# Kernel tuning notes

Hardware: AMD Instinct MI355X
Metric: run time of the kernel (lower is better)

## Reference

```python
import jax, jax.numpy as jnp
import numpy as np
from jax import lax

DIM = 2048
HEAD_DIM = 128
N_HEADS = 16
N_KV_HEADS = 4
N_REP = N_HEADS // N_KV_HEADS
K_CHUNK = 8          # token_chunk
SEQ = 2048
BATCH = 1
ROPE_THETA = 10000.0
KV_DIM = N_KV_HEADS * HEAD_DIM  # 512


def _make_freq_cis(seq, hd, theta):
    # (seq, hd//2, 2, 2) rotation matrices [[cos, -sin], [sin, cos]]
    inv = 1.0 / (theta ** (np.arange(0, hd, 2, dtype=np.float64) / hd))
    ang = np.outer(np.arange(seq, dtype=np.float64), inv)
    cos, sin = np.cos(ang), np.sin(ang)
    f = np.stack([np.stack([cos, -sin], -1), np.stack([sin, cos], -1)], -2)
    return jnp.asarray(f, jnp.float32)


def setup_inputs() -> dict:
    key = jax.random.key(0)
    ks = jax.random.split(key, 12)
    s = 0.02
    inp = {
        'x': jax.random.normal(ks[0], (BATCH, SEQ, DIM), jnp.float32),
        'freq_cis': _make_freq_cis(SEQ, HEAD_DIM, ROPE_THETA),
        # nn.Linear weights stored as (out, in); y = x @ W.T
        'wq': jax.random.normal(ks[1], (N_HEADS * HEAD_DIM, DIM), jnp.float32) * s,
        'wk': jax.random.normal(ks[2], (KV_DIM, DIM), jnp.float32) * s,
        'wv': jax.random.normal(ks[3], (KV_DIM, DIM), jnp.float32) * s,
        'wo': jax.random.normal(ks[4], (DIM, N_HEADS * HEAD_DIM), jnp.float32) * s,
        # diagonal SSM params for k_ssm / v_ssm (per-channel)
        'a_log_k': jax.random.normal(ks[5], (KV_DIM,), jnp.float32) * 0.5,
        'b_k': jax.random.normal(ks[6], (KV_DIM,), jnp.float32),
        'c_k': jax.random.normal(ks[7], (KV_DIM,), jnp.float32),
        'a_log_v': jax.random.normal(ks[8], (KV_DIM,), jnp.float32) * 0.5,
        'b_v': jax.random.normal(ks[9], (KV_DIM,), jnp.float32),
        'c_v': jax.random.normal(ks[10], (KV_DIM,), jnp.float32),
    }
    return inp


def _ssm_chunked(x, a_log, b, c):
    # Chunked diagonal SSM with state reset every K_CHUNK tokens
    # (equivalent to flat_process_chunks_with_ssm with boundaries every K).
    bsz, S, E = x.shape
    nc = S // K_CHUNK
    a = jnp.exp(-jax.nn.softplus(a_log))  # (E,) decay in (0, 1)
    xs = x.reshape(bsz * nc, K_CHUNK, E).swapaxes(0, 1)  # (K, N, E)

    def step(h, xt):
        h = a * h + b * xt
        return h, c * h

    _, ys = lax.scan(step, jnp.zeros((bsz * nc, E), x.dtype), xs)
    return ys.swapaxes(0, 1).reshape(bsz, S, E)


def _apply_rope(xq, xk, freq_cis):
    # xq: (b, s, h, hd); freq_cis: (s, hd//2, 2, 2)
    def rot(t):
        b, s, h, hd = t.shape
        tr = t.reshape(b, s, h, hd // 2, 1, 2)
        f = freq_cis.reshape(1, s, 1, hd // 2, 2, 2)
        return (tr * f).sum(-1).reshape(b, s, h, hd)
    return rot(xq), rot(xk)


def _forward(x, freq_cis, wq, wk, wv, wo, a_log_k, b_k, c_k, a_log_v, b_v, c_v):
    bsz, S, _ = x.shape
    xq = jnp.einsum('bsd,ed->bse', x, wq)
    xk = jnp.einsum('bsd,ed->bse', x, wk)
    xv = jnp.einsum('bsd,ed->bse', x, wv)

    # chunked SSM preprocessing of K/V (+ residual_ssm)
    xk_p = _ssm_chunked(xk, a_log_k, b_k, c_k) + xk
    xv_p = _ssm_chunked(xv, a_log_v, b_v, c_v) + xv

    xq = xq.reshape(bsz, S, N_HEADS, HEAD_DIM)
    xk_p = xk_p.reshape(bsz, S, N_KV_HEADS, HEAD_DIM)
    xv_p = xv_p.reshape(bsz, S, N_KV_HEADS, HEAD_DIM)

    xq, xk_p = _apply_rope(xq, xk_p, freq_cis)

    # GQA repeat_kv (torch.repeat_interleave on head dim)
    xk_p = jnp.repeat(xk_p, N_REP, axis=2)
    xv_p = jnp.repeat(xv_p, N_REP, axis=2)

    # chunk-boundary attention mask
    k_pos = jnp.arange(S)
    boundary = (k_pos % K_CHUNK) == (K_CHUNK - 1)
    t = jnp.arange(S)[:, None]
    k = k_pos[None, :]
    mask = ((k < t) & boundary[None, :]) | (k == t - 1) | ((k < 4) & (k <= t))

    q = xq.transpose(0, 2, 1, 3)   # (b, h, s, d)
    kk = xk_p.transpose(0, 2, 1, 3)
    vv = xv_p.transpose(0, 2, 1, 3)

    scores = jnp.einsum('bhqd,bhkd->bhqk', q, kk) / jnp.sqrt(
        jnp.asarray(HEAD_DIM, q.dtype))
    scores = jnp.where(mask[None, None], scores, -jnp.inf)
    attn = jax.nn.softmax(scores, axis=-1)
    out = jnp.einsum('bhqk,bhkd->bhqd', attn, vv)
    out = out.transpose(0, 2, 1, 3).reshape(bsz, S, N_HEADS * HEAD_DIM)
    return jnp.einsum('bse,de->bsd', out, wo)


def reference(x, freq_cis, wq, wk, wv, wo, a_log_k, b_k, c_k,
              a_log_v, b_v, c_v):
    return _forward(x, freq_cis, wq, wk, wv, wo,
                    a_log_k, b_k, c_k, a_log_v, b_v, c_v)
```

## Files before the change

kernel.cpp:

```cpp
#include <hip/hip_runtime.h>

typedef __bf16 bf16x8 __attribute__((ext_vector_type(8)));
typedef float  f32x4  __attribute__((ext_vector_type(4)));
typedef unsigned short u16;
typedef unsigned int   u32;

__device__ __forceinline__ float b2f(u16 u) {
    u32 x = ((u32)u) << 16;
    return __builtin_bit_cast(float, x);
}
__device__ __forceinline__ u16 f2b(float f) {
    u32 x = __builtin_bit_cast(u32, f);
    x += 0x7fffu + ((x >> 16) & 1u);
    return (u16)(x >> 16);
}

__global__ void convert_kernel(const float* __restrict__ x, const float* __restrict__ wq,
                               const float* __restrict__ wk, const float* __restrict__ wv,
                               const float* __restrict__ wo,
                               u16* __restrict__ xb, u16* __restrict__ wcat, u16* __restrict__ wob)
{
    long i4 = (long)blockIdx.x * 256 + threadIdx.x;
    long e = i4 * 4;
    const float* src; u16* dst;
    if (e < 4194304) { src = x + e; dst = xb + e; }
    else if (e < 10485760) {
        long j = e - 4194304;
        dst = wcat + j;
        if (j < 4194304)      src = wq + j;
        else if (j < 5242880) src = wk + (j - 4194304);
        else                  src = wv + (j - 5242880);
    } else {
        long j = e - 10485760;
        src = wo + j; dst = wob + j;
    }
    float4 v = *(const float4*)src;
    uint2 pk;
    pk.x = (u32)f2b(v.x) | ((u32)f2b(v.y) << 16);
    pk.y = (u32)f2b(v.z) | ((u32)f2b(v.w) << 16);
    *(uint2*)dst = pk;
}

template<int MODE>
__global__ __launch_bounds__(256) void gemm_bt128_kernel(
    const u16* __restrict__ A, const u16* __restrict__ B,
    void* __restrict__ Cout, int M, int N, int K,
    u16* __restrict__ qb, u16* __restrict__ c1kv, const float* __restrict__ fc)
{
    __shared__ u16 As[2][8192];
    __shared__ u16 Bs[2][8192];
    const int tid  = threadIdx.x;
    const int lane = tid & 63;
    const int wave = tid >> 6;
    const int waveM = wave >> 1, waveN = wave & 1;
    const int tm = blockIdx.y * 128;
    const int tn = blockIdx.x * 128;

    f32x4 acc[4][4];
#pragma unroll
    for (int i = 0; i < 4; ++i)
#pragma unroll
        for (int j = 0; j < 4; ++j) acc[i][j] = f32x4{0.f, 0.f, 0.f, 0.f};

    const int frow = lane & 15;
    const int fk   = (lane >> 4) * 8;

    auto STAGE = [&](int buf, int kt) {
#pragma unroll
        for (int c = 0; c < 4; ++c) {
            int idx = c * 256 + tid;
            int row = idx >> 3;
            int blk = (idx & 7) ^ (row & 7);
            const u16* srcA = A + (size_t)(tm + row) * K + kt + blk * 8;
            u16* dstA = &As[buf][(size_t)(c * 256 + wave * 64) * 8];
            __builtin_amdgcn_global_load_lds((const __attribute__((address_space(1))) void*)srcA,
                                             (__attribute__((address_space(3))) void*)dstA, 16, 0, 0);
        }
#pragma unroll
        for (int c = 0; c < 4; ++c) {
            int idx = c * 256 + tid;
            int row = idx >> 3;
            int blk = (idx & 7) ^ (row & 7);
            const u16* srcB = B + (size_t)(tn + row) * K + kt + blk * 8;
            u16* dstB = &Bs[buf][(size_t)(c * 256 + wave * 64) * 8];
            __builtin_amdgcn_global_load_lds((const __attribute__((address_space(1))) void*)srcB,
                                             (__attribute__((address_space(3))) void*)dstB, 16, 0, 0);
        }
    };
    auto COMPUTE = [&](int buf) {
#pragma unroll
        for (int kk = 0; kk < 64; kk += 32) {
            bf16x8 af[4], bfr[4];
#pragma unroll
            for (int m = 0; m < 4; ++m) {
                int r  = waveM * 64 + m * 16 + frow;
                int kb_ = ((kk + fk) >> 3) ^ (r & 7);
                af[m] = *(const bf16x8*)&As[buf][r * 64 + kb_ * 8];
            }
#pragma unroll
            for (int n = 0; n < 4; ++n) {
                int r  = waveN * 64 + n * 16 + frow;
                int kb_ = ((kk + fk) >> 3) ^ (r & 7);
                bfr[n] = *(const bf16x8*)&Bs[buf][r * 64 + kb_ * 8];
            }
#pragma unroll
            for (int m = 0; m < 4; ++m)
#pragma unroll
                for (int n = 0; n < 4; ++n)
                    acc[m][n] = __builtin_amdgcn_mfma_f32_16x16x32_bf16(af[m], bfr[n], acc[m][n], 0, 0, 0);
        }
    };

    const int nk = K >> 6;
    STAGE(0, 0);
    int buf = 0;
    for (int t = 0; t < nk - 1; ++t) {
        STAGE(buf ^ 1, (t + 1) << 6);
        asm volatile("s_waitcnt vmcnt(8)" ::: "memory");
        __builtin_amdgcn_s_barrier();
        __builtin_amdgcn_sched_barrier(0);
        COMPUTE(buf);
        __builtin_amdgcn_sched_barrier(0);
        __builtin_amdgcn_s_barrier();
        buf ^= 1;
    }
    asm volatile("s_waitcnt vmcnt(0)" ::: "memory");
    __builtin_amdgcn_s_barrier();
    __builtin_amdgcn_sched_barrier(0);
    COMPUTE(buf);

    const int rb = tm + waveM * 64;
    const int cb = tn + waveN * 64;
    const int s  = lane & 15;
    if (MODE == 0) {
#pragma unroll
        for (int m = 0; m < 4; ++m)
#pragma unroll
            for (int n = 0; n < 4; ++n)
#pragma unroll
                for (int r = 0; r < 4; ++r) {
                    int row = rb + m * 16 + (lane >> 4) * 4 + r;
                    int col = cb + n * 16 + s;
                    ((float*)Cout)[(size_t)row * N + col] = acc[m][n][r];
                }
    } else if (tn < 2048) {
#pragma unroll
        for (int m = 0; m < 4; ++m)
#pragma unroll
            for (int n = 0; n < 4; ++n)
#pragma unroll
                for (int r = 0; r < 4; ++r) {
                    int row = rb + m * 16 + (lane >> 4) * 4 + r;
                    int col = cb + n * 16 + s;
                    float val  = acc[m][n][r];
                    float part = __shfl_xor(val, 1);
                    int i = (col & 127) >> 1;
                    const float* f4 = &fc[((size_t)row * 64 + i) * 4];
                    float cs = f4[0], sn = f4[2];
                    float q = (s & 1) ? (part * sn + val * cs)
                                      : (val * cs - part * sn);
                    qb[(size_t)row * 2048 + col] = f2b(q);
                }
    } else {
#pragma unroll
        for (int m = 0; m < 4; ++m)
#pragma unroll
            for (int n = 0; n < 4; ++n)
#pragma unroll
                for (int r = 0; r < 4; ++r) {
                    int row = rb + m * 16 + (lane >> 4) * 4 + r;
                    int col = cb + n * 16 + s;
                    c1kv[(size_t)row * 1024 + (col - 2048)] = f2b(acc[m][n][r]);
                }
    }
}

__global__ __launch_bounds__(256) void gemm_bt_kernel(
    const u16* __restrict__ A, const u16* __restrict__ B,
    float* __restrict__ Cout, int M, int N, int K)
{
    __shared__ u16 As[2][8192];
    __shared__ u16 Bs[2][4096];
    const int tid  = threadIdx.x;
    const int lane = tid & 63;
    const int wave = tid >> 6;
    const int waveM = wave >> 1, waveN = wave & 1;
    const int tm = blockIdx.y * 128;
    const int tn = blockIdx.x * 64;

    f32x4 acc[4][2];
#pragma unroll
    for (int i = 0; i < 4; ++i)
#pragma unroll
        for (int j = 0; j < 2; ++j) acc[i][j] = f32x4{0.f, 0.f, 0.f, 0.f};

    const int frow = lane & 15;
    const int fk   = (lane >> 4) * 8;

    auto STAGE = [&](int buf, int kt) {
#pragma unroll
        for (int c = 0; c < 4; ++c) {
            int idx = c * 256 + tid;
            int row = idx >> 3;
            int blk = (idx & 7) ^ (row & 7);
            const u16* srcA = A + (size_t)(tm + row) * K + kt + blk * 8;
            u16* dstA = &As[buf][(size_t)(c * 256 + wave * 64) * 8];
            __builtin_amdgcn_global_load_lds((const __attribute__((address_space(1))) void*)srcA,
                                             (__attribute__((address_space(3))) void*)dstA, 16, 0, 0);
        }
#pragma unroll
        for (int c = 0; c < 2; ++c) {
            int idx = c * 256 + tid;
            int row = idx >> 3;
            int blk = (idx & 7) ^ (row & 7);
            const u16* srcB = B + (size_t)(tn + row) * K + kt + blk * 8;
            u16* dstB = &Bs[buf][(size_t)(c * 256 + wave * 64) * 8];
            __builtin_amdgcn_global_load_lds((const __attribute__((address_space(1))) void*)srcB,
                                             (__attribute__((address_space(3))) void*)dstB, 16, 0, 0);
        }
    };
    auto COMPUTE = [&](int buf) {
#pragma unroll
        for (int kk = 0; kk < 64; kk += 32) {
            bf16x8 af[4], bfr[2];
#pragma unroll
            for (int m = 0; m < 4; ++m) {
                int r  = waveM * 64 + m * 16 + frow;
                int kb_ = ((kk + fk) >> 3) ^ (r & 7);
                af[m] = *(const bf16x8*)&As[buf][r * 64 + kb_ * 8];
            }
#pragma unroll
            for (int n = 0; n < 2; ++n) {
                int r  = waveN * 32 + n * 16 + frow;
                int kb_ = ((kk + fk) >> 3) ^ (r & 7);
                bfr[n] = *(const bf16x8*)&Bs[buf][r * 64 + kb_ * 8];
            }
#pragma unroll
            for (int m = 0; m < 4; ++m)
#pragma unroll
                for (int n = 0; n < 2; ++n)
                    acc[m][n] = __builtin_amdgcn_mfma_f32_16x16x32_bf16(af[m], bfr[n], acc[m][n], 0, 0, 0);
        }
    };

    const int nk = K >> 6;
    STAGE(0, 0);
    int buf = 0;
    for (int t = 0; t < nk - 1; ++t) {
        STAGE(buf ^ 1, (t + 1) << 6);
        asm volatile("s_waitcnt vmcnt(6)" ::: "memory");
        __builtin_amdgcn_s_barrier();
        __builtin_amdgcn_sched_barrier(0);
        COMPUTE(buf);
        __builtin_amdgcn_sched_barrier(0);
        __builtin_amdgcn_s_barrier();
        buf ^= 1;
    }
    asm volatile("s_waitcnt vmcnt(0)" ::: "memory");
    __builtin_amdgcn_s_barrier();
    __builtin_amdgcn_sched_barrier(0);
    COMPUTE(buf);

    const int rb = tm + waveM * 64;
    const int cb = tn + waveN * 32;
#pragma unroll
    for (int m = 0; m < 4; ++m)
#pragma unroll
        for (int n = 0; n < 2; ++n)
#pragma unroll
            for (int r = 0; r < 4; ++r) {
                int row = rb + m * 16 + (lane >> 4) * 4 + r;
                int col = cb + n * 16 + (lane & 15);
                Cout[(size_t)row * N + col] = acc[m][n][r];
            }
}

__global__ void ssm_kv_kernel(const u16* __restrict__ c1kv, const float* __restrict__ fc,
                              const float* __restrict__ alk, const float* __restrict__ bk,
                              const float* __restrict__ ck,
                              const float* __restrict__ alv, const float* __restrict__ bv,
                              const float* __restrict__ cv,
                              u16* __restrict__ kb, u16* __restrict__ vb,
                              u16* __restrict__ kbc, u16* __restrict__ vbt)
{
    int gi = blockIdx.x * 256 + threadIdx.x;
    if (gi < 65536) {
        int chunk = gi >> 8, pr = gi & 255;
        int i = pr & 63;
        int e0 = (pr >> 6) * 128 + 2 * i;
        float z0 = alk[e0], z1 = alk[e0 + 1];
        float sp0 = z0 > 20.f ? z0 : log1pf(__expf(z0));
        float sp1 = z1 > 20.f ? z1 : log1pf(__expf(z1));
        float a0 = __expf(-sp0), a1 = __expf(-sp1);
        float b0 = bk[e0], b1 = bk[e0 + 1];
        float c0 = ck[e0], cc1 = ck[e0 + 1];
        float h0 = 0.f, h1 = 0.f;
        int kvh = e0 >> 7, d = e0 & 127;
#pragma unroll
        for (int tt = 0; tt < 8; ++tt) {
            int sr = chunk * 8 + tt;
            u32 u = *(const u32*)&c1kv[(size_t)sr * 1024 + e0];
            float x0 = b2f((u16)(u & 0xffff)), x1 = b2f((u16)(u >> 16));
            h0 = a0 * h0 + b0 * x0;
            h1 = a1 * h1 + b1 * x1;
            float y0 = c0 * h0 + x0;
            float y1 = cc1 * h1 + x1;
            const float* f4 = &fc[((size_t)sr * 64 + i) * 4];
            float k0 = y0 * f4[0] - y1 * f4[2];
            float k1 = y0 * f4[2] + y1 * f4[0];
            u32 pk = (u32)f2b(k0) | ((u32)f2b(k1) << 16);
            *(u32*)&kb[(size_t)sr * 512 + e0] = pk;
            if (tt == 7)
                *(u32*)&kbc[(size_t)kvh * 32768 + chunk * 128 + d] = pk;
        }
    } else {
        int vi = gi - 65536;
        int chunk = vi >> 9, e = vi & 511;
        float z = alv[e];
        float sp = z > 20.f ? z : log1pf(__expf(z));
        float a = __expf(-sp);
        float b = bv[e], c = cv[e];
        float h = 0.f;
#pragma unroll
        for (int tt = 0; tt < 8; ++tt) {
            int sr = chunk * 8 + tt;
            float xvv = b2f(c1kv[(size_t)sr * 1024 + 512 + e]);
            h = a * h + b * xvv;
            u16 y = f2b(c * h + xvv);
            vb[(size_t)sr * 512 + e] = y;
            if (tt == 7)
                vbt[((size_t)e << 8) + chunk] = y;
        }
    }
}

__global__ __launch_bounds__(512, 2) void attn_kernel(
    const u16* __restrict__ qb, const u16* __restrict__ kb, const u16* __restrict__ vb,
    const u16* __restrict__ kbc, const u16* __restrict__ vbt, u16* __restrict__ aout)
{
    __shared__ u16   ksbuf[32768];
    __shared__ u16   vsbuf[32768];
    __shared__ float p_ext[8][16][32];

    const int tid  = threadIdx.x;
    const int w    = tid >> 6;
    const int lane = tid & 63;
    const int s    = lane & 15;
    const int g    = lane >> 4;
    const int h    = blockIdx.x >> 4;
    const int t0   = (blockIdx.x & 15) * 128;
    const int kvh  = h >> 2;
    const int qw   = t0 + w * 16;

    {
        const u16* kcb = kbc + ((size_t)kvh << 15);
#pragma unroll
        for (int it = 0; it < 8; ++it) {
            int idx = it * 512 + tid;
            int r = idx >> 4, b = idx & 15;
            const u16* src = kcb + r * 128 + ((b ^ (r & 7)) << 3);
            u16* dst = ksbuf + (size_t)(it * 512 + w * 64) * 8;
            __builtin_amdgcn_global_load_lds((const __attribute__((address_space(1))) void*)src,
                                             (__attribute__((address_space(3))) void*)dst, 16, 0, 0);
        }
    }
    __syncthreads();

    {
        const u16* vtb = vbt + ((size_t)kvh << 15);
#pragma unroll
        for (int it = 0; it < 8; ++it) {
            int idx = it * 512 + tid;
            int r = idx >> 5, b = idx & 31;
            const u16* src = vtb + r * 256 + ((b ^ (r & 7)) << 3);
            u16* dst = vsbuf + (size_t)(it * 512 + w * 64) * 8;
            __builtin_amdgcn_global_load_lds((const __attribute__((address_space(1))) void*)src,
                                             (__attribute__((address_space(3))) void*)dst, 16, 0, 0);
        }
    }

    bf16x8 qa[4];
    {
        const u16* qr = qb + (size_t)(qw + s) * 2048 + h * 128 + g * 8;
#pragma unroll
        for (int kk = 0; kk < 4; ++kk) qa[kk] = *(const bf16x8*)&qr[kk * 32];
    }

    f32x4 sf[18];
#pragma unroll
    for (int i = 0; i < 18; ++i) sf[i] = f32x4{0.f, 0.f, 0.f, 0.f};

#pragma unroll
    for (int fb = 0; fb < 16; ++fb) {
        int row = fb * 16 + s;
#pragma unroll
        for (int kk = 0; kk < 4; ++kk) {
            int ch = (kk * 4 + g) ^ (s & 7);
            bf16x8 bf = *(const bf16x8*)&ksbuf[row * 128 + ch * 8];
            sf[fb] = __builtin_amdgcn_mfma_f32_16x16x32_bf16(qa[kk], bf, sf[fb], 0, 0, 0);
        }
    }
#pragma unroll
    for (int xb = 0; xb < 2; ++xb) {
        int i = xb * 16 + s;
        int keyrow = (i < 4) ? i : (qw + (i - 4) - 1);
        if (keyrow < 0) keyrow = 0;
        if (keyrow > 2047) keyrow = 2047;
        const u16* kr = kb + (size_t)keyrow * 512 + kvh * 128 + g * 8;
#pragma unroll
        for (int kk = 0; kk < 4; ++kk) {
            bf16x8 bf = *(const bf16x8*)&kr[kk * 32];
            sf[16 + xb] = __builtin_amdgcn_mfma_f32_16x16x32_bf16(qa[kk], bf, sf[16 + xb], 0, 0, 0);
        }
    }

    const float scale = 0.08838834764831845f;
    float mx[4] = {-1e30f, -1e30f, -1e30f, -1e30f};
#pragma unroll
    for (int fi = 0; fi < 18; ++fi)
#pragma unroll
        for (int r = 0; r < 4; ++r) {
            int q = g * 4 + r;
            int t = qw + q;
            bool ok;
            if (fi < 16) {
                int j = fi * 16 + s;
                ok = j < (t >> 3);
            } else {
                int i = (fi - 16) * 16 + s;
                if (i < 4) ok = (i <= t);
                else       ok = ((i - 4) == q) && ((t & 7) != 0) && (t >= 5);
            }
            float v = ok ? sf[fi][r] * scale : -1e30f;
            sf[fi][r] = v;
            mx[r] = fmaxf(mx[r], v);
        }
#pragma unroll
    for (int r = 0; r < 4; ++r)
#pragma unroll
        for (int off = 8; off; off >>= 1) mx[r] = fmaxf(mx[r], __shfl_xor(mx[r], off));

    float sm[4] = {0.f, 0.f, 0.f, 0.f};
#pragma unroll
    for (int fi = 0; fi < 18; ++fi)
#pragma unroll
        for (int r = 0; r < 4; ++r) {
            float p = __expf(sf[fi][r] - mx[r]);
            sf[fi][r] = p;
            sm[r] += p;
        }
#pragma unroll
    for (int r = 0; r < 4; ++r)
#pragma unroll
        for (int off = 8; off; off >>= 1) sm[r] += __shfl_xor(sm[r], off);
    float inv[4];
#pragma unroll
    for (int r = 0; r < 4; ++r) inv[r] = 1.f / sm[r];

    __syncthreads();

    u16* pbuf = ksbuf + w * 4096;
#pragma unroll
    for (int fi = 0; fi < 16; ++fi)
#pragma unroll
        for (int r = 0; r < 4; ++r) {
            int q = g * 4 + r;
            int c = fi * 16 + s;
            int blk = (c >> 3) ^ q;
            pbuf[q * 256 + (blk << 3) + (c & 7)] = f2b(sf[fi][r]);
        }
#pragma unroll
    for (int xb = 0; xb < 2; ++xb)
#pragma unroll
        for (int r = 0; r < 4; ++r)
            p_ext[w][g * 4 + r][xb * 16 + s] = sf[16 + xb][r];

    bf16x8 pa[8];
#pragma unroll
    for (int kk = 0; kk < 8; ++kk) {
        int blk = (kk * 4 + g) ^ s;
        pa[kk] = *(const bf16x8*)&pbuf[s * 256 + (blk << 3)];
    }
    f32x4 out[8];
#pragma unroll
    for (int f = 0; f < 8; ++f) out[f] = f32x4{0.f, 0.f, 0.f, 0.f};
#pragma unroll
    for (int f = 0; f < 8; ++f) {
        int row = f * 16 + s;
#pragma unroll
        for (int kk = 0; kk < 8; ++kk) {
            int ch = (kk * 4 + g) ^ (s & 7);
            bf16x8 vf = *(const bf16x8*)&vsbuf[row * 256 + ch * 8];
            out[f] = __builtin_amdgcn_mfma_f32_16x16x32_bf16(pa[kk], vf, out[f], 0, 0, 0);
        }
    }

    {
        float v4[4][8];
#pragma unroll
        for (int e = 0; e < 4; ++e)
#pragma unroll
            for (int f = 0; f < 8; ++f)
                v4[e][f] = b2f(vb[(size_t)e * 512 + kvh * 128 + f * 16 + s]);
#pragma unroll
        for (int r = 0; r < 4; ++r) {
            int q = g * 4 + r;
            int t = qw + q;
#pragma unroll
            for (int e = 0; e < 4; ++e) {
                float p = p_ext[w][q][e];
#pragma unroll
                for (int f = 0; f < 8; ++f) out[f][r] += p * v4[e][f];
            }
            float pp = p_ext[w][q][4 + q];
            int key = t - 1; if (key < 0) key = 0;
            const u16* vr = vb + (size_t)key * 512 + kvh * 128;
#pragma unroll
            for (int f = 0; f < 8; ++f) out[f][r] += pp * b2f(vr[f * 16 + s]);
        }
    }

#pragma unroll
    for (int f = 0; f < 8; ++f)
#pragma unroll
        for (int r = 0; r < 4; ++r) {
            int t = qw + g * 4 + r;
            aout[(size_t)t * 2048 + h * 128 + f * 16 + s] = f2b(out[f][r] * inv[r]);
        }
}

extern "C" void kernel_launch(void* const* d_in, const int* in_sizes, int n_in,
                              void* d_out, int out_size, void* d_ws, size_t ws_size,
                              hipStream_t stream) {
    const float* x   = (const float*)d_in[0];
    const float* fc  = (const float*)d_in[1];
    const float* wq  = (const float*)d_in[2];
    const float* wk  = (const float*)d_in[3];
    const float* wv  = (const float*)d_in[4];
    const float* wo  = (const float*)d_in[5];
    const float* alk = (const float*)d_in[6];
    const float* bk  = (const float*)d_in[7];
    const float* ck  = (const float*)d_in[8];
    const float* alv = (const float*)d_in[9];
    const float* bv  = (const float*)d_in[10];
    const float* cv  = (const float*)d_in[11];

    char* ws = (char*)d_ws;
    u16*   xb   = (u16*)(ws);
    u16*   wcat = (u16*)(ws + 8388608);
    u16*   wob  = (u16*)(ws + 20971520);
    u16*   c1kv = (u16*)(ws + 29360128);
    u16*   qb   = (u16*)(ws + 54525952);
    u16*   kb   = (u16*)(ws + 62914560);
    u16*   vb   = (u16*)(ws + 65011712);
    u16*   kbc  = (u16*)(ws + 67108864);
    u16*   vbt  = (u16*)(ws + 67371008);
    u16*   aout = (u16*)(ws + 67633152);

    convert_kernel<<<14336, 256, 0, stream>>>(x, wq, wk, wv, wo, xb, wcat, wob);

    dim3 g1(3072 / 128, 2048 / 128);
    gemm_bt128_kernel<1><<<g1, 256, 0, stream>>>(xb, wcat, nullptr, 2048, 3072, 2048,
                                                 qb, c1kv, fc);

    ssm_kv_kernel<<<768, 256, 0, stream>>>(c1kv, fc, alk, bk, ck, alv, bv, cv,
                                           kb, vb, kbc, vbt);

    attn_kernel<<<256, 512, 0, stream>>>(qb, kb, vb, kbc, vbt, aout);

    dim3 g3(2048 / 64, 2048 / 128);
    gemm_bt_kernel<<<g3, 256, 0, stream>>>(aout, wob, (float*)d_out, 2048, 2048, 2048);
}
```

Baseline: 110.1 us.

## Narrow QKV GEMM tiles and triple-buffer output GEMM with single barrier

The fused QKV projection GEMM now uses 128x64 tiles instead of 128x128, doubling the block count so the grid covers the CUs more evenly. The cost is lower per-block data reuse and extra A-tile traffic. The output projection GEMM moves from a double-buffered loop with two barriers per iteration to a three-stage LDS ring with one barrier. This keeps one tile load in flight during compute, at the price of more shared memory per block.

Result: faster. 102.1 us (median of 2 runs) (-7.3%).

```diff
diff --git a/kernel.cpp b/kernel.cpp
--- a/kernel.cpp
+++ b/kernel.cpp
@@ -41,26 +41,25 @@
     *(uint2*)dst = pk;
 }
 
-template<int MODE>
-__global__ __launch_bounds__(256) void gemm_bt128_kernel(
+__global__ __launch_bounds__(256) void gemm_qkv_kernel(
     const u16* __restrict__ A, const u16* __restrict__ B,
-    void* __restrict__ Cout, int M, int N, int K,
+    int M, int N, int K,
     u16* __restrict__ qb, u16* __restrict__ c1kv, const float* __restrict__ fc)
 {
     __shared__ u16 As[2][8192];
-    __shared__ u16 Bs[2][8192];
+    __shared__ u16 Bs[2][4096];
     const int tid  = threadIdx.x;
     const int lane = tid & 63;
     const int wave = tid >> 6;
     const int waveM = wave >> 1, waveN = wave & 1;
     const int tm = blockIdx.y * 128;
-    const int tn = blockIdx.x * 128;
-
-    f32x4 acc[4][4];
+    const int tn = blockIdx.x * 64;
+
+    f32x4 acc[4][2];
 #pragma unroll
     for (int i = 0; i < 4; ++i)
 #pragma unroll
-        for (int j = 0; j < 4; ++j) acc[i][j] = f32x4{0.f, 0.f, 0.f, 0.f};
+        for (int j = 0; j < 2; ++j) acc[i][j] = f32x4{0.f, 0.f, 0.f, 0.f};
 
     const int frow = lane & 15;
     const int fk   = (lane >> 4) * 8;
@@ -77,7 +76,7 @@
                                              (__attribute__((address_space(3))) void*)dstA, 16, 0, 0);
         }
 #pragma unroll
-        for (int c = 0; c < 4; ++c) {
+        for (int c = 0; c < 2; ++c) {
             int idx = c * 256 + tid;
             int row = idx >> 3;
             int blk = (idx & 7) ^ (row & 7);
@@ -90,7 +89,7 @@
     auto COMPUTE = [&](int buf) {
 #pragma unroll
         for (int kk = 0; kk < 64; kk += 32) {
-            bf16x8 af[4], bfr[4];
+            bf16x8 af[4], bfr[2];
 #pragma unroll
             for (int m = 0; m < 4; ++m) {
                 int r  = waveM * 64 + m * 16 + frow;
@@ -98,15 +97,15 @@
                 af[m] = *(const bf16x8*)&As[buf][r * 64 + kb_ * 8];
             }
 #pragma unroll
-            for (int n = 0; n < 4; ++n) {
-                int r  = waveN * 64 + n * 16 + frow;
+            for (int n = 0; n < 2; ++n) {
+                int r  = waveN * 32 + n * 16 + frow;
                 int kb_ = ((kk + fk) >> 3) ^ (r & 7);
                 bfr[n] = *(const bf16x8*)&Bs[buf][r * 64 + kb_ * 8];
             }
 #pragma unroll
             for (int m = 0; m < 4; ++m)
 #pragma unroll
-                for (int n = 0; n < 4; ++n)
+                for (int n = 0; n < 2; ++n)
                     acc[m][n] = __builtin_amdgcn_mfma_f32_16x16x32_bf16(af[m], bfr[n], acc[m][n], 0, 0, 0);
         }
     };
@@ -116,7 +115,7 @@
     int buf = 0;
     for (int t = 0; t < nk - 1; ++t) {
         STAGE(buf ^ 1, (t + 1) << 6);
-        asm volatile("s_waitcnt vmcnt(8)" ::: "memory");
+        asm volatile("s_waitcnt vmcnt(6)" ::: "memory");
         __builtin_amdgcn_s_barrier();
         __builtin_amdgcn_sched_barrier(0);
         COMPUTE(buf);
@@ -130,24 +129,13 @@
     COMPUTE(buf);
 
     const int rb = tm + waveM * 64;
-    const int cb = tn + waveN * 64;
+    const int cb = tn + waveN * 32;
     const int s  = lane & 15;
-    if (MODE == 0) {
+    if (tn < 2048) {
 #pragma unroll
         for (int m = 0; m < 4; ++m)
 #pragma unroll
-            for (int n = 0; n < 4; ++n)
-#pragma unroll
-                for (int r = 0; r < 4; ++r) {
-                    int row = rb + m * 16 + (lane >> 4) * 4 + r;
-                    int col = cb + n * 16 + s;
-                    ((float*)Cout)[(size_t)row * N + col] = acc[m][n][r];
-                }
-    } else if (tn < 2048) {
-#pragma unroll
-        for (int m = 0; m < 4; ++m)
-#pragma unroll
-            for (int n = 0; n < 4; ++n)
+            for (int n = 0; n < 2; ++n)
 #pragma unroll
                 for (int r = 0; r < 4; ++r) {
                     int row = rb + m * 16 + (lane >> 4) * 4 + r;
@@ -165,7 +153,7 @@
 #pragma unroll
         for (int m = 0; m < 4; ++m)
 #pragma unroll
-            for (int n = 0; n < 4; ++n)
+            for (int n = 0; n < 2; ++n)
 #pragma unroll
                 for (int r = 0; r < 4; ++r) {
                     int row = rb + m * 16 + (lane >> 4) * 4 + r;
@@ -175,12 +163,12 @@
     }
 }
 
-__global__ __launch_bounds__(256) void gemm_bt_kernel(
+__global__ __launch_bounds__(256) void gemm_out_kernel(
     const u16* __restrict__ A, const u16* __restrict__ B,
     float* __restrict__ Cout, int M, int N, int K)
 {
-    __shared__ u16 As[2][8192];
-    __shared__ u16 Bs[2][4096];
+    __shared__ u16 As[3][8192];
+    __shared__ u16 Bs[3][4096];
     const int tid  = threadIdx.x;
     const int lane = tid & 63;
     const int wave = tid >> 6;
@@ -245,21 +233,23 @@
 
     const int nk = K >> 6;
     STAGE(0, 0);
-    int buf = 0;
-    for (int t = 0; t < nk - 1; ++t) {
-        STAGE(buf ^ 1, (t + 1) << 6);
+    STAGE(1, 64);
+    for (int t = 0; t < nk - 2; ++t) {
         asm volatile("s_waitcnt vmcnt(6)" ::: "memory");
         __builtin_amdgcn_s_barrier();
         __builtin_amdgcn_sched_barrier(0);
-        COMPUTE(buf);
+        STAGE((t + 2) % 3, (t + 2) << 6);
+        COMPUTE(t % 3);
         __builtin_amdgcn_sched_barrier(0);
-        __builtin_amdgcn_s_barrier();
-        buf ^= 1;
-    }
+    }
+    asm volatile("s_waitcnt vmcnt(6)" ::: "memory");
+    __builtin_amdgcn_s_barrier();
+    __builtin_amdgcn_sched_barrier(0);
+    COMPUTE((nk - 2) % 3);
     asm volatile("s_waitcnt vmcnt(0)" ::: "memory");
     __builtin_amdgcn_s_barrier();
     __builtin_amdgcn_sched_barrier(0);
-    COMPUTE(buf);
+    COMPUTE((nk - 1) % 3);
 
     const int rb = tm + waveM * 64;
     const int cb = tn + waveN * 32;
@@ -559,9 +549,9 @@
 
     convert_kernel<<<14336, 256, 0, stream>>>(x, wq, wk, wv, wo, xb, wcat, wob);
 
-    dim3 g1(3072 / 128, 2048 / 128);
-    gemm_bt128_kernel<1><<<g1, 256, 0, stream>>>(xb, wcat, nullptr, 2048, 3072, 2048,
-                                                 qb, c1kv, fc);
+    dim3 g1(3072 / 64, 2048 / 128);
+    gemm_qkv_kernel<<<g1, 256, 0, stream>>>(xb, wcat, 2048, 3072, 2048,
+                                            qb, c1kv, fc);
 
     ssm_kv_kernel<<<768, 256, 0, stream>>>(c1kv, fc, alk, bk, ck, alv, bv, cv,
                                            kb, vb, kbc, vbt);
@@ -569,5 +559,5 @@
     attn_kernel<<<256, 512, 0, stream>>>(qb, kb, vb, kbc, vbt, aout);
 
     dim3 g3(2048 / 64, 2048 / 128);
-    gemm_bt_kernel<<<g3, 256, 0, stream>>>(aout, wob, (float*)d_out, 2048, 2048, 2048);
-}
+    gemm_out_kernel<<<g3, 256, 0, stream>>>(aout, wob, (float*)d_out, 2048, 2048, 2048);
+}
```
